# Kernel optimization log

Hardware: AMD Instinct MI355X
Metric: run time of the kernel (lower is better)

## Reference

```python
import jax, jax.numpy as jnp
import numpy as np

H = 256
L = 5
B = 1024
NL, EL = 65536, 262144
NP_, EP = 131072, 524288
BN_EPS = 1e-5


def _bn_relu(x, gamma, beta):
    # BatchNorm1d (training mode, biased variance) followed by ReLU
    m = x.mean(axis=0)
    v = ((x - m) ** 2).mean(axis=0)
    return jax.nn.relu((x - m) * jax.lax.rsqrt(v + BN_EPS) * gamma + beta)


def _gin_conv(h, src, dst, W1, b1, W2, b2):
    # GINConv, eps=0: mlp(x + sum_{j->i} x_j)
    agg = jax.ops.segment_sum(h[src], dst, num_segments=h.shape[0])
    z = h + agg
    return jax.nn.relu(z @ W1 + b1) @ W2 + b2


def _forward(lig_x, prot_x, lig_embed_W, lig_embed_b, prot_embed_W, prot_embed_b,
             lig_virtual0, prot_virtual0,
             lig_conv_W1, lig_conv_b1, lig_conv_W2, lig_conv_b2,
             lig_vmlp_W, lig_vmlp_b, lig_vmlp_gamma, lig_vmlp_beta,
             prot_conv_W1, prot_conv_b1, prot_conv_W2, prot_conv_b2,
             prot_vmlp_W, prot_vmlp_b, prot_vmlp_gamma, prot_vmlp_beta,
             pred_W1, pred_b1, pred_W2, pred_b2,
             lig_batch, prot_batch, lig_edge_index, prot_edge_index):
    lig_h = lig_x @ lig_embed_W + lig_embed_b        # [NL, H]
    prot_h = prot_x @ prot_embed_W + prot_embed_b    # [NP, H]
    lig_v = jnp.broadcast_to(lig_virtual0, (B, H))
    prot_v = jnp.broadcast_to(prot_virtual0, (B, H))
    l_src, l_dst = lig_edge_index[0], lig_edge_index[1]
    p_src, p_dst = prot_edge_index[0], prot_edge_index[1]
    for i in range(L):
        # ligand branch: virtual-node pool -> MLP -> broadcast, then GIN conv (residual)
        lig_v = lig_v + jax.ops.segment_sum(lig_h, lig_batch, num_segments=B)
        lig_v = _bn_relu(lig_v @ lig_vmlp_W[i] + lig_vmlp_b[i], lig_vmlp_gamma[i], lig_vmlp_beta[i])
        lig_h = lig_h + lig_v[lig_batch]
        lig_h = lig_h + _gin_conv(lig_h, l_src, l_dst, lig_conv_W1[i], lig_conv_b1[i], lig_conv_W2[i], lig_conv_b2[i])
        # protein branch
        prot_v = prot_v + jax.ops.segment_sum(prot_h, prot_batch, num_segments=B)
        prot_v = _bn_relu(prot_v @ prot_vmlp_W[i] + prot_vmlp_b[i], prot_vmlp_gamma[i], prot_vmlp_beta[i])
        prot_h = prot_h + prot_v[prot_batch]
        prot_h = prot_h + _gin_conv(prot_h, p_src, p_dst, prot_conv_W1[i], prot_conv_b1[i], prot_conv_W2[i], prot_conv_b2[i])
    lig_cnt = jax.ops.segment_sum(jnp.ones((lig_h.shape[0],), lig_h.dtype), lig_batch, num_segments=B)
    prot_cnt = jax.ops.segment_sum(jnp.ones((prot_h.shape[0],), prot_h.dtype), prot_batch, num_segments=B)
    lig_pool = jax.ops.segment_sum(lig_h, lig_batch, num_segments=B) / lig_cnt[:, None]
    prot_pool = jax.ops.segment_sum(prot_h, prot_batch, num_segments=B) / prot_cnt[:, None]
    combined = jnp.concatenate([lig_pool, prot_pool], axis=-1)  # [B, 2H]
    return jax.nn.relu(combined @ pred_W1 + pred_b1) @ pred_W2 + pred_b2  # [B, 1]


def setup_inputs() -> dict:
    key = jax.random.key(0)
    ks = jax.random.split(key, 40)
    s = 0.05
    inp = {
        'lig_x': jax.random.normal(ks[0], (NL, 26), jnp.float32),
        'prot_x': jax.random.normal(ks[1], (NP_, 20), jnp.float32),
        'lig_embed_W': jax.random.normal(ks[2], (26, H), jnp.float32) * s,
        'lig_embed_b': jnp.zeros((H,), jnp.float32),
        'prot_embed_W': jax.random.normal(ks[3], (20, H), jnp.float32) * s,
        'prot_embed_b': jnp.zeros((H,), jnp.float32),
        'lig_virtual0': jax.random.normal(ks[4], (1, H), jnp.float32),
        'prot_virtual0': jax.random.normal(ks[5], (1, H), jnp.float32),
        'lig_conv_W1': jax.random.normal(ks[6], (L, H, H), jnp.float32) * s,
        'lig_conv_b1': jnp.zeros((L, H), jnp.float32),
        'lig_conv_W2': jax.random.normal(ks[7], (L, H, H), jnp.float32) * s,
        'lig_conv_b2': jnp.zeros((L, H), jnp.float32),
        'lig_vmlp_W': jax.random.normal(ks[8], (L, H, H), jnp.float32) * s,
        'lig_vmlp_b': jnp.zeros((L, H), jnp.float32),
        'lig_vmlp_gamma': jnp.ones((L, H), jnp.float32),
        'lig_vmlp_beta': jnp.zeros((L, H), jnp.float32),
        'prot_conv_W1': jax.random.normal(ks[9], (L, H, H), jnp.float32) * s,
        'prot_conv_b1': jnp.zeros((L, H), jnp.float32),
        'prot_conv_W2': jax.random.normal(ks[10], (L, H, H), jnp.float32) * s,
        'prot_conv_b2': jnp.zeros((L, H), jnp.float32),
        'prot_vmlp_W': jax.random.normal(ks[11], (L, H, H), jnp.float32) * s,
        'prot_vmlp_b': jnp.zeros((L, H), jnp.float32),
        'prot_vmlp_gamma': jnp.ones((L, H), jnp.float32),
        'prot_vmlp_beta': jnp.zeros((L, H), jnp.float32),
        'pred_W1': jax.random.normal(ks[12], (2 * H, H), jnp.float32) * s,
        'pred_b1': jnp.zeros((H,), jnp.float32),
        'pred_W2': jax.random.normal(ks[13], (H, 1), jnp.float32) * s,
        'pred_b2': jnp.zeros((1,), jnp.float32),
        # sorted batch ids covering all B graphs (PyG-style contiguous batching)
        'lig_batch': (jnp.arange(NL, dtype=jnp.int32) * B) // NL,
        'prot_batch': (jnp.arange(NP_, dtype=jnp.int32) * B) // NP_,
        'lig_edge_index': jax.random.randint(ks[14], (2, EL), 0, NL, jnp.int32),
        'prot_edge_index': jax.random.randint(ks[15], (2, EP), 0, NP_, jnp.int32),
    }
    return inp


def reference(lig_x, prot_x, lig_embed_W, lig_embed_b, prot_embed_W, prot_embed_b,
              lig_virtual0, prot_virtual0,
              lig_conv_W1, lig_conv_b1, lig_conv_W2, lig_conv_b2,
              lig_vmlp_W, lig_vmlp_b, lig_vmlp_gamma, lig_vmlp_beta,
              prot_conv_W1, prot_conv_b1, prot_conv_W2, prot_conv_b2,
              prot_vmlp_W, prot_vmlp_b, prot_vmlp_gamma, prot_vmlp_beta,
              pred_W1, pred_b1, pred_W2, pred_b2,
              lig_batch, prot_batch, lig_edge_index, prot_edge_index):
    return _forward(lig_x, prot_x, lig_embed_W, lig_embed_b, prot_embed_W, prot_embed_b,
                    lig_virtual0, prot_virtual0,
                    lig_conv_W1, lig_conv_b1, lig_conv_W2, lig_conv_b2,
                    lig_vmlp_W, lig_vmlp_b, lig_vmlp_gamma, lig_vmlp_beta,
                    prot_conv_W1, prot_conv_b1, prot_conv_W2, prot_conv_b2,
                    prot_vmlp_W, prot_vmlp_b, prot_vmlp_gamma, prot_vmlp_beta,
                    pred_W1, pred_b1, pred_W2, pred_b2,
                    lig_batch, prot_batch, lig_edge_index, prot_edge_index)
```

## Files before the change

### kernel.cpp

```cpp
#include <hip/hip_runtime.h>

#define H_DIM 256
#define NLAYER 5
#define BGRAPH 1024
#define CAP 24

typedef __attribute__((ext_vector_type(8))) short short8;
typedef __attribute__((ext_vector_type(4))) float f32x4;

struct __align__(8) us4 { unsigned short x, y, z, w; };

__device__ __forceinline__ float b2f(unsigned short u) {
    union { float f; unsigned v; } c; c.v = ((unsigned)u) << 16; return c.f;
}
__device__ __forceinline__ unsigned short f2b(float f) {
    union { float f; unsigned v; } c; c.f = f;
    return (unsigned short)((c.v + 0x7fffu + ((c.v >> 16) & 1u)) >> 16);
}

__global__ __launch_bounds__(256) void embed_kernel(
    const float* __restrict__ x, const float* __restrict__ W,
    const float* __restrict__ b, unsigned short* __restrict__ h, int K)
{
    __shared__ float xs[256];
    const int m0 = blockIdx.x * 8;
    const int tid = threadIdx.x;
    if (tid < 8 * K) xs[tid] = x[(size_t)m0 * K + tid];
    __syncthreads();
    const int n = tid;
    float acc[8] = {0.f,0.f,0.f,0.f,0.f,0.f,0.f,0.f};
    for (int k = 0; k < K; ++k) {
        const float w = W[k * H_DIM + n];
        #pragma unroll
        for (int r = 0; r < 8; ++r) acc[r] += xs[r * K + k] * w;
    }
    const float bb = b[n];
    #pragma unroll
    for (int r = 0; r < 8; ++r)
        h[(size_t)(m0 + r) * H_DIM + n] = f2b(acc[r] + bb);
}

__global__ __launch_bounds__(256) void init_v_kernel(
    const float* __restrict__ lig0, const float* __restrict__ prot0,
    float* __restrict__ lig_v, float* __restrict__ prot_v)
{
    const int b = blockIdx.x, n = threadIdx.x;
    lig_v[b * H_DIM + n]  = lig0[n];
    prot_v[b * H_DIM + n] = prot0[n];
}

__global__ __launch_bounds__(64) void wprep_kernel(
    const float* __restrict__ W, unsigned short* __restrict__ Wf)
{
    const int kb = blockIdx.x, nb = blockIdx.y, l = blockIdx.z;
    const int lane = threadIdx.x, q = lane >> 4, l15 = lane & 15;
    const float* Wl = W + (size_t)l * 65536;
    unsigned short* dst = Wf + (size_t)l * 65536
                        + ((size_t)(kb * 16 + nb) * 64 + lane) * 8;
    const int kbase = kb * 32 + q * 8;
    const int n = nb * 16 + l15;
    us4 o0, o1;
    o0.x = f2b(Wl[(size_t)(kbase + 0) * 256 + n]);
    o0.y = f2b(Wl[(size_t)(kbase + 1) * 256 + n]);
    o0.z = f2b(Wl[(size_t)(kbase + 2) * 256 + n]);
    o0.w = f2b(Wl[(size_t)(kbase + 3) * 256 + n]);
    o1.x = f2b(Wl[(size_t)(kbase + 4) * 256 + n]);
    o1.y = f2b(Wl[(size_t)(kbase + 5) * 256 + n]);
    o1.z = f2b(Wl[(size_t)(kbase + 6) * 256 + n]);
    o1.w = f2b(Wl[(size_t)(kbase + 7) * 256 + n]);
    *(us4*)dst = o0;
    *(us4*)(dst + 4) = o1;
}

__global__ __launch_bounds__(256) void bucket_build_kernel(
    const int* __restrict__ src, const int* __restrict__ dst, int E,
    int* __restrict__ deg, int* __restrict__ bucket)
{
    const int e = blockIdx.x * 256 + threadIdx.x;
    if (e >= E) return;
    const int d = dst[e], s = src[e];
    const int slot = atomicAdd(&deg[d], 1);
    if (slot < CAP) bucket[(size_t)d * CAP + slot] = s;
}

__global__ __launch_bounds__(256) void pool0_kernel(
    const unsigned short* __restrict__ hL, const unsigned short* __restrict__ hP,
    float* __restrict__ hsL, float* __restrict__ hsP)
{
    const int br = blockIdx.y, b = blockIdx.x, n = threadIdx.x;
    const unsigned short* h = br ? hP : hL;
    float* hs = br ? hsP : hsL;
    const int cnt = br ? 128 : 64;
    const unsigned short* hp = &h[(size_t)b * cnt * H_DIM + n];
    float s = 0.f;
    #pragma unroll 8
    for (int r = 0; r < cnt; ++r) s += b2f(hp[(size_t)r * H_DIM]);
    hs[(size_t)b * H_DIM + n] = s;
}

__global__ __launch_bounds__(256) void vmlp_gemm_kernel(
    const float* __restrict__ vL, const float* __restrict__ hsL,
    const float* __restrict__ WL, const float* __restrict__ bL,
    const float* __restrict__ vP, const float* __restrict__ hsP,
    const float* __restrict__ WP, const float* __restrict__ bP,
    float* __restrict__ vtL, float* __restrict__ vtP,
    float* __restrict__ part)
{
    constexpr int BM = 32, BN = 64, BK = 32, TM = 2, K = H_DIM, N = H_DIM;
    __shared__ __align__(16) float As[BK][BM + 4];
    __shared__ __align__(16) float Bs[BK][BN];
    __shared__ float st[2][64];
    const int br = blockIdx.z;
    const float* v    = br ? vP  : vL;
    const float* hsum = br ? hsP : hsL;
    const float* W    = br ? WP  : WL;
    const float* bias = br ? bP  : bL;
    float* vt = br ? vtP : vtL;
    float* pt = part + br * 512;
    const int tid = threadIdx.x;
    const int tx = tid & 15;
    const int ty = tid >> 4;
    const int m0 = blockIdx.x * BM;
    const int n0 = blockIdx.y * BN;

    float acc[TM][4] = {};

    for (int kt = 0; kt < K; kt += BK) {
        {
            const int row = tid >> 3, kq = tid & 7;
            const size_t ao = (size_t)(m0 + row) * K + kt + kq * 4;
            float4 a = *(const float4*)&v[ao];
            const float4 h4 = *(const float4*)&hsum[ao];
            a.x += h4.x; a.y += h4.y; a.z += h4.z; a.w += h4.w;
            As[kq * 4 + 0][row] = a.x;
            As[kq * 4 + 1][row] = a.y;
            As[kq * 4 + 2][row] = a.z;
            As[kq * 4 + 3][row] = a.w;
        }
        #pragma unroll
        for (int i = 0; i < 2; ++i) {
            const int f = tid + i * 256;
            const int row = f >> 4, c4 = f & 15;
            *(float4*)&Bs[row][c4 * 4] =
                *(const float4*)&W[(size_t)(kt + row) * N + n0 + c4 * 4];
        }
        __syncthreads();
        #pragma unroll
        for (int kk = 0; kk < BK; ++kk) {
            const float4 bv = *(const float4*)&Bs[kk][tx * 4];
            #pragma unroll
            for (int im = 0; im < TM; ++im) {
                const float a = As[kk][ty * TM + im];
                acc[im][0] += a * bv.x; acc[im][1] += a * bv.y;
                acc[im][2] += a * bv.z; acc[im][3] += a * bv.w;
            }
        }
        __syncthreads();
    }

    if (tid < 128) ((float*)st)[tid] = 0.f;
    __syncthreads();

    const float4 bb = *(const float4*)&bias[n0 + tx * 4];
    float cs[4] = {0.f,0.f,0.f,0.f}, cq[4] = {0.f,0.f,0.f,0.f};
    #pragma unroll
    for (int im = 0; im < TM; ++im) {
        const int m = m0 + ty * TM + im;
        float4 r;
        r.x = acc[im][0] + bb.x; r.y = acc[im][1] + bb.y;
        r.z = acc[im][2] + bb.z; r.w = acc[im][3] + bb.w;
        *(float4*)&vt[(size_t)m * N + n0 + tx * 4] = r;
        cs[0] += r.x; cq[0] += r.x * r.x;
        cs[1] += r.y; cq[1] += r.y * r.y;
        cs[2] += r.z; cq[2] += r.z * r.z;
        cs[3] += r.w; cq[3] += r.w * r.w;
    }
    #pragma unroll
    for (int c = 0; c < 4; ++c) {
        atomicAdd(&st[0][tx * 4 + c], cs[c]);
        atomicAdd(&st[1][tx * 4 + c], cq[c]);
    }
    __syncthreads();
    if (tid < 64) {
        atomicAdd(&pt[n0 + tid], st[0][tid]);
        atomicAdd(&pt[256 + n0 + tid], st[1][tid]);
    }
}

__global__ __launch_bounds__(256) void vmlp_apply_kernel(
    const float* __restrict__ part,
    const float* __restrict__ gL, const float* __restrict__ beL,
    const float* __restrict__ gP, const float* __restrict__ beP,
    const float* __restrict__ vtL, const float* __restrict__ vtP,
    float* __restrict__ vL, float* __restrict__ vP)
{
    const int br = blockIdx.y, n = threadIdx.x;
    const float* pt = part + br * 512;
    const float* g  = br ? gP  : gL;
    const float* be = br ? beP : beL;
    const float* vt = br ? vtP : vtL;
    float* v = br ? vP : vL;
    const float s  = pt[n];
    const float s2 = pt[256 + n];
    const float mean = s * (1.f / BGRAPH);
    const float var  = s2 * (1.f / BGRAPH) - mean * mean;
    const float sc = g[n] * rsqrtf(var + 1e-5f);
    const float sh = be[n] - mean * sc;
    #pragma unroll
    for (int r = 0; r < 4; ++r) {
        const size_t i = (size_t)(blockIdx.x * 4 + r) * H_DIM + n;
        v[i] = fmaxf(vt[i] * sc + sh, 0.f);
    }
}

__global__ __launch_bounds__(512) void conv_fused3_kernel(
    const unsigned short* __restrict__ Hin,
    const int* __restrict__ deg, const int* __restrict__ bucket,
    const int* __restrict__ batch, const float* __restrict__ v,
    const unsigned short* __restrict__ Wf1, const float* __restrict__ b1,
    const unsigned short* __restrict__ Wf2, const float* __restrict__ b2,
    unsigned short* __restrict__ Hout, float* __restrict__ hsum)
{
    __shared__ __align__(16) unsigned short U[64 * 256];
    __shared__ float hl[256];
    char* Ub = (char*)U;
    const int tid  = threadIdx.x;
    const int lane = tid & 63;
    const int wid  = tid >> 6;
    const int wr   = wid >> 2;
    const int wc   = wid & 3;
    const int q    = lane >> 4;
    const int l15  = lane & 15;
    const int m0   = blockIdx.x * 64;
    const int bq0  = batch[m0];
    const float* __restrict__ vg = v + (size_t)bq0 * H_DIM;

    if (tid < 256) hl[tid] = 0.f;

    {
        const float4 vm = *(const float4*)&vg[lane * 4];
        for (int r8 = 0; r8 < 8; ++r8) {
            const int lr = wid * 8 + r8;
            const int m = m0 + lr;
            const us4 hv = *(const us4*)&Hin[(size_t)m * H_DIM + lane * 4];
            float4 acc = { b2f(hv.x) + vm.x, b2f(hv.y) + vm.y,
                           b2f(hv.z) + vm.z, b2f(hv.w) + vm.w };
            int cnt = deg[m]; if (cnt > CAP) cnt = CAP;
            const int* bp = &bucket[(size_t)m * CAP];
            for (int i = 0; i < cnt; i += 4) {
                const int4 s4 = *(const int4*)&bp[i];
                const int rem = cnt - i;
                us4 a0, a1, a2, a3;
                int q0, q1, q2, q3;
                a0 = *(const us4*)&Hin[(size_t)s4.x * H_DIM + lane * 4];
                q0 = batch[s4.x];
                if (rem > 1) { a1 = *(const us4*)&Hin[(size_t)s4.y * H_DIM + lane * 4]; q1 = batch[s4.y]; }
                if (rem > 2) { a2 = *(const us4*)&Hin[(size_t)s4.z * H_DIM + lane * 4]; q2 = batch[s4.z]; }
                if (rem > 3) { a3 = *(const us4*)&Hin[(size_t)s4.w * H_DIM + lane * 4]; q3 = batch[s4.w]; }
                {
                    const float4 w0 = *(const float4*)&v[(size_t)q0 * H_DIM + lane * 4];
                    acc.x += b2f(a0.x) + w0.x; acc.y += b2f(a0.y) + w0.y;
                    acc.z += b2f(a0.z) + w0.z; acc.w += b2f(a0.w) + w0.w;
                }
                if (rem > 1) {
                    const float4 w1 = *(const float4*)&v[(size_t)q1 * H_DIM + lane * 4];
                    acc.x += b2f(a1.x) + w1.x; acc.y += b2f(a1.y) + w1.y;
                    acc.z += b2f(a1.z) + w1.z; acc.w += b2f(a1.w) + w1.w;
                }
                if (rem > 2) {
                    const float4 w2 = *(const float4*)&v[(size_t)q2 * H_DIM + lane * 4];
                    acc.x += b2f(a2.x) + w2.x; acc.y += b2f(a2.y) + w2.y;
                    acc.z += b2f(a2.z) + w2.z; acc.w += b2f(a2.w) + w2.w;
                }
                if (rem > 3) {
                    const float4 w3 = *(const float4*)&v[(size_t)q3 * H_DIM + lane * 4];
                    acc.x += b2f(a3.x) + w3.x; acc.y += b2f(a3.y) + w3.y;
                    acc.z += b2f(a3.z) + w3.z; acc.w += b2f(a3.w) + w3.w;
                }
            }
            us4 o = { f2b(acc.x), f2b(acc.y), f2b(acc.z), f2b(acc.w) };
            const int ab = lr * 512 + ((lane * 8) ^ ((lr & 7) << 4));
            *(us4*)(Ub + ab) = o;
        }
    }
    __syncthreads();

    f32x4 acc[2][4];
    #pragma unroll
    for (int i = 0; i < 2; ++i)
        #pragma unroll
        for (int j = 0; j < 4; ++j) acc[i][j] = (f32x4){0.f, 0.f, 0.f, 0.f};

    const int arow = wr * 32 + l15;
    const int rowb0 = arow * 512;
    const int rowb1 = rowb0 + 16 * 512;
    const int xorv = (l15 & 7) << 4;
    const unsigned short* wb1 = Wf1 + ((size_t)(wc * 4) * 64 + lane) * 8;
    const unsigned short* wb2 = Wf2 + ((size_t)(wc * 4) * 64 + lane) * 8;

    #pragma unroll 2
    for (int kb = 0; kb < 8; ++kb) {
        const int c0 = (kb * 64 + q * 16) ^ xorv;
        const short8 av0 = *(const short8*)(Ub + rowb0 + c0);
        const short8 av1 = *(const short8*)(Ub + rowb1 + c0);
        #pragma unroll
        for (int ni = 0; ni < 4; ++ni) {
            const short8 bv = *(const short8*)&wb1[(size_t)kb * 8192 + ni * 512];
            acc[0][ni] = __builtin_amdgcn_mfma_f32_16x16x32_bf16(av0, bv, acc[0][ni], 0, 0, 0);
            acc[1][ni] = __builtin_amdgcn_mfma_f32_16x16x32_bf16(av1, bv, acc[1][ni], 0, 0, 0);
        }
    }
    __syncthreads();

    #pragma unroll
    for (int ni = 0; ni < 4; ++ni) {
        const int col = wc * 64 + ni * 16 + l15;
        const float bb = b1[col];
        #pragma unroll
        for (int mi = 0; mi < 2; ++mi)
            #pragma unroll
            for (int j = 0; j < 4; ++j) {
                const int row = wr * 32 + mi * 16 + q * 4 + j;
                const int tb = row * 512 + ((col * 2) ^ ((row & 7) << 4));
                *(unsigned short*)(Ub + tb) = f2b(fmaxf(acc[mi][ni][j] + bb, 0.f));
            }
    }
    #pragma unroll
    for (int i = 0; i < 2; ++i)
        #pragma unroll
        for (int j = 0; j < 4; ++j) acc[i][j] = (f32x4){0.f, 0.f, 0.f, 0.f};
    __syncthreads();

    #pragma unroll 2
    for (int kb = 0; kb < 8; ++kb) {
        const int c0 = (kb * 64 + q * 16) ^ xorv;
        const short8 av0 = *(const short8*)(Ub + rowb0 + c0);
        const short8 av1 = *(const short8*)(Ub + rowb1 + c0);
        #pragma unroll
        for (int ni = 0; ni < 4; ++ni) {
            const short8 bv = *(const short8*)&wb2[(size_t)kb * 8192 + ni * 512];
            acc[0][ni] = __builtin_amdgcn_mfma_f32_16x16x32_bf16(av0, bv, acc[0][ni], 0, 0, 0);
            acc[1][ni] = __builtin_amdgcn_mfma_f32_16x16x32_bf16(av1, bv, acc[1][ni], 0, 0, 0);
        }
    }

    int cols[4]; float b2c[4], vc[4];
    #pragma unroll
    for (int ni = 0; ni < 4; ++ni) {
        cols[ni] = wc * 64 + ni * 16 + l15;
        b2c[ni] = b2[cols[ni]];
        vc[ni]  = vg[cols[ni]];
    }
    float lsum[4] = {0.f, 0.f, 0.f, 0.f};
    #pragma unroll
    for (int mi = 0; mi < 2; ++mi)
        #pragma unroll
        for (int j = 0; j < 4; ++j) {
            const int row = m0 + wr * 32 + mi * 16 + q * 4 + j;
            const unsigned short* hip_ = &Hin[(size_t)row * H_DIM];
            unsigned short* hop = &Hout[(size_t)row * H_DIM];
            #pragma unroll
            for (int ni = 0; ni < 4; ++ni) {
                const float val = b2f(hip_[cols[ni]]) + vc[ni]
                                + acc[mi][ni][j] + b2c[ni];
                hop[cols[ni]] = f2b(val);
                lsum[ni] += val;
            }
        }
    #pragma unroll
    for (int ni = 0; ni < 4; ++ni) atomicAdd(&hl[cols[ni]], lsum[ni]);
    __syncthreads();
    if (tid < 256) atomicAdd(&hsum[(size_t)bq0 * H_DIM + tid], hl[tid]);
}

template<bool RELU>
__global__ __launch_bounds__(256) void gemm_small_kernel(
    const float* __restrict__ A, const float* __restrict__ W,
    const float* __restrict__ bias, float* __restrict__ C,
    int M, int N, int K)
{
    constexpr int BM = 32, BN = 64, BK = 32, TM = 2;
    __shared__ __align__(16) float As[BK][BM + 4];
    __shared__ __align__(16) float Bs[BK][BN];
    const int tid = threadIdx.x;
    const int tx = tid & 15;
    const int ty = tid >> 4;
    const int m0 = blockIdx.x * BM;
    const int n0 = blockIdx.y * BN;

    float acc[TM][4] = {};

    for (int kt = 0; kt < K; kt += BK) {
        {
            const int row = tid >> 3, kq = tid & 7;
            const float4 a = *(const float4*)&A[(size_t)(m0 + row) * K + kt + kq * 4];
            As[kq * 4 + 0][row] = a.x;
            As[kq * 4 + 1][row] = a.y;
            As[kq * 4 + 2][row] = a.z;
            As[kq * 4 + 3][row] = a.w;
        }
        #pragma unroll
        for (int i = 0; i < 2; ++i) {
            const int f = tid + i * 256;
            const int row = f >> 4, c4 = f & 15;
            *(float4*)&Bs[row][c4 * 4] =
                *(const float4*)&W[(size_t)(kt + row) * N + n0 + c4 * 4];
        }
        __syncthreads();
        #pragma unroll
        for (int kk = 0; kk < BK; ++kk) {
            const float4 bv = *(const float4*)&Bs[kk][tx * 4];
            #pragma unroll
            for (int im = 0; im < TM; ++im) {
                const float a = As[kk][ty * TM + im];
                acc[im][0] += a * bv.x; acc[im][1] += a * bv.y;
                acc[im][2] += a * bv.z; acc[im][3] += a * bv.w;
            }
        }
        __syncthreads();
    }

    const float4 bb = *(const float4*)&bias[n0 + tx * 4];
    #pragma unroll
    for (int im = 0; im < TM; ++im) {
        const int m = m0 + ty * TM + im;
        float4 r;
        r.x = acc[im][0] + bb.x; r.y = acc[im][1] + bb.y;
        r.z = acc[im][2] + bb.z; r.w = acc[im][3] + bb.w;
        if constexpr (RELU) {
            r.x = fmaxf(r.x, 0.f); r.y = fmaxf(r.y, 0.f);
            r.z = fmaxf(r.z, 0.f); r.w = fmaxf(r.w, 0.f);
        }
        *(float4*)&C[(size_t)m * N + n0 + tx * 4] = r;
    }
}

__global__ __launch_bounds__(256) void pool_hsum_kernel(
    const float* __restrict__ hl, const float* __restrict__ hp,
    float* __restrict__ comb)
{
    const int b = blockIdx.x, n = threadIdx.x;
    comb[(size_t)b * 512 + n]       = hl[(size_t)b * H_DIM + n] * (1.f / 64.f);
    comb[(size_t)b * 512 + 256 + n] = hp[(size_t)b * H_DIM + n] * (1.f / 128.f);
}

__global__ __launch_bounds__(256) void pred_final_kernel(
    const float* __restrict__ hidden, const float* __restrict__ W2,
    const float* __restrict__ b2, float* __restrict__ out)
{
    const int b = blockIdx.x, t = threadIdx.x;
    float p = hidden[(size_t)b * H_DIM + t] * W2[t];
    #pragma unroll
    for (int off = 32; off >= 1; off >>= 1) p += __shfl_down(p, off);
    __shared__ float red[4];
    if ((t & 63) == 0) red[t >> 6] = p;
    __syncthreads();
    if (t == 0) out[b] = red[0] + red[1] + red[2] + red[3] + b2[0];
}

extern "C" void kernel_launch(void* const* d_in, const int* in_sizes, int n_in,
                              void* d_out, int out_size, void* d_ws, size_t ws_size,
                              hipStream_t stream)
{
    const int NL = 65536, NP = 131072, EL = 262144, EP = 524288;
    const int B = BGRAPH, H = H_DIM;

    const float* lig_x        = (const float*)d_in[0];
    const float* prot_x       = (const float*)d_in[1];
    const float* lig_embed_W  = (const float*)d_in[2];
    const float* lig_embed_b  = (const float*)d_in[3];
    const float* prot_embed_W = (const float*)d_in[4];
    const float* prot_embed_b = (const float*)d_in[5];
    const float* lig_virtual0 = (const float*)d_in[6];
    const float* prot_virtual0= (const float*)d_in[7];
    const float* lig_conv_W1  = (const float*)d_in[8];
    const float* lig_conv_b1  = (const float*)d_in[9];
    const float* lig_conv_W2  = (const float*)d_in[10];
    const float* lig_conv_b2  = (const float*)d_in[11];
    const float* lig_vmlp_W   = (const float*)d_in[12];
    const float* lig_vmlp_b   = (const float*)d_in[13];
    const float* lig_vmlp_g   = (const float*)d_in[14];
    const float* lig_vmlp_be  = (const float*)d_in[15];
    const float* prot_conv_W1 = (const float*)d_in[16];
    const float* prot_conv_b1 = (const float*)d_in[17];
    const float* prot_conv_W2 = (const float*)d_in[18];
    const float* prot_conv_b2 = (const float*)d_in[19];
    const float* prot_vmlp_W  = (const float*)d_in[20];
    const float* prot_vmlp_b  = (const float*)d_in[21];
    const float* prot_vmlp_g  = (const float*)d_in[22];
    const float* prot_vmlp_be = (const float*)d_in[23];
    const float* pred_W1      = (const float*)d_in[24];
    const float* pred_b1      = (const float*)d_in[25];
    const float* pred_W2      = (const float*)d_in[26];
    const float* pred_b2      = (const float*)d_in[27];
    const int* lig_batch      = (const int*)d_in[28];
    const int* prot_batch     = (const int*)d_in[29];
    const int* lig_ei         = (const int*)d_in[30];
    const int* prot_ei        = (const int*)d_in[31];

    float* ws = (float*)d_ws;
    float* lig_v    = ws;
    float* prot_v   = lig_v    + (size_t)B * H;
    float* vtmpL    = prot_v   + (size_t)B * H;
    float* vtmpP    = vtmpL    + (size_t)B * H;
    float* part     = vtmpP    + (size_t)B * H;
    float* comb     = part     + 1024;
    float* hidden   = comb     + (size_t)B * 2 * H;
    float* hsum_lig = hidden   + (size_t)B * H;
    float* hsum_prot= hsum_lig + (size_t)B * H;
    unsigned short* lig_h0  = (unsigned short*)(hsum_prot + (size_t)B * H);
    unsigned short* lig_h1  = lig_h0  + (size_t)NL * H;
    unsigned short* prot_h0 = lig_h1  + (size_t)NL * H;
    unsigned short* prot_h1 = prot_h0 + (size_t)NP * H;
    unsigned short* wf_lw1  = prot_h1 + (size_t)NP * H;
    unsigned short* wf_lw2  = wf_lw1 + (size_t)NLAYER * H * H;
    unsigned short* wf_pw1  = wf_lw2 + (size_t)NLAYER * H * H;
    unsigned short* wf_pw2  = wf_pw1 + (size_t)NLAYER * H * H;
    int* deg_lig  = (int*)(wf_pw2 + (size_t)NLAYER * H * H);
    int* deg_prot = deg_lig  + NL;
    int* bkt_lig  = deg_prot + NP;
    int* bkt_prot = bkt_lig  + (size_t)NL * CAP;

    hipMemsetAsync(deg_lig, 0, (size_t)(NL + NP) * sizeof(int), stream);
    bucket_build_kernel<<<EL / 256, 256, 0, stream>>>(
        lig_ei, lig_ei + EL, EL, deg_lig, bkt_lig);
    bucket_build_kernel<<<EP / 256, 256, 0, stream>>>(
        prot_ei, prot_ei + EP, EP, deg_prot, bkt_prot);
    wprep_kernel<<<dim3(8, 16, NLAYER), 64, 0, stream>>>(lig_conv_W1, wf_lw1);
    wprep_kernel<<<dim3(8, 16, NLAYER), 64, 0, stream>>>(lig_conv_W2, wf_lw2);
    wprep_kernel<<<dim3(8, 16, NLAYER), 64, 0, stream>>>(prot_conv_W1, wf_pw1);
    wprep_kernel<<<dim3(8, 16, NLAYER), 64, 0, stream>>>(prot_conv_W2, wf_pw2);

    embed_kernel<<<NL / 8, 256, 0, stream>>>(lig_x, lig_embed_W, lig_embed_b, lig_h0, 26);
    embed_kernel<<<NP / 8, 256, 0, stream>>>(prot_x, prot_embed_W, prot_embed_b, prot_h0, 20);
    init_v_kernel<<<B, 256, 0, stream>>>(lig_virtual0, prot_virtual0, lig_v, prot_v);
    pool0_kernel<<<dim3(B, 2), 256, 0, stream>>>(lig_h0, prot_h0, hsum_lig, hsum_prot);

    for (int i = 0; i < NLAYER; ++i) {
        const size_t wo = (size_t)i * H * H;
        const size_t bo = (size_t)i * H;
        unsigned short* lin  = (i & 1) ? lig_h1  : lig_h0;
        unsigned short* lout = (i & 1) ? lig_h0  : lig_h1;
        unsigned short* pin  = (i & 1) ? prot_h1 : prot_h0;
        unsigned short* pout = (i & 1) ? prot_h0 : prot_h1;

        hipMemsetAsync(part, 0, 1024 * sizeof(float), stream);
        vmlp_gemm_kernel<<<dim3(32, 4, 2), 256, 0, stream>>>(
            lig_v, hsum_lig, lig_vmlp_W + wo, lig_vmlp_b + bo,
            prot_v, hsum_prot, prot_vmlp_W + wo, prot_vmlp_b + bo,
            vtmpL, vtmpP, part);
        vmlp_apply_kernel<<<dim3(256, 2), 256, 0, stream>>>(
            part, lig_vmlp_g + bo, lig_vmlp_be + bo,
            prot_vmlp_g + bo, prot_vmlp_be + bo,
            vtmpL, vtmpP, lig_v, prot_v);
        hipMemsetAsync(hsum_lig, 0, (size_t)2 * B * H * sizeof(float), stream);
        conv_fused3_kernel<<<NL / 64, 512, 0, stream>>>(
            lin, deg_lig, bkt_lig, lig_batch, lig_v,
            wf_lw1 + wo, lig_conv_b1 + bo, wf_lw2 + wo, lig_conv_b2 + bo,
            lout, hsum_lig);
        conv_fused3_kernel<<<NP / 64, 512, 0, stream>>>(
            pin, deg_prot, bkt_prot, prot_batch, prot_v,
            wf_pw1 + wo, prot_conv_b1 + bo, wf_pw2 + wo, prot_conv_b2 + bo,
            pout, hsum_prot);
    }

    pool_hsum_kernel<<<B, 256, 0, stream>>>(hsum_lig, hsum_prot, comb);
    gemm_small_kernel<true><<<dim3(B / 32, 4), 256, 0, stream>>>(
        comb, pred_W1, pred_b1, hidden, B, H, 2 * H);
    pred_final_kernel<<<B, 256, 0, stream>>>(hidden, pred_W2, pred_b2, (float*)d_out);
}
```

Baseline: 1.823 ms.

## Shrink conv tile to 32 rows and interleave two-row neighbor gathers

The fused GIN conv kernel now processes 32 rows per block with 256 threads instead of 64 rows with 512. Each wave owns all 32 rows and a 64-column slice of the MFMA output, and LDS use drops by half. The gather phase handles two destination rows at once so their neighbor loads are issued together, aiming for more memory-level parallelism on the random gathers. The cost is twice as many blocks, twice as many hsum atomics, and weight tiles reloaded per block for half as many rows, which may add pressure on L2.

Result: faster. 1.755 ms (-3.7%).

```diff
diff --git a/kernel.cpp b/kernel.cpp
--- a/kernel.cpp
+++ b/kernel.cpp
@@ -213,7 +213,7 @@
     }
 }
 
-__global__ __launch_bounds__(512) void conv_fused3_kernel(
+__global__ __launch_bounds__(256) void conv_fused4_kernel(
     const unsigned short* __restrict__ Hin,
     const int* __restrict__ deg, const int* __restrict__ bucket,
     const int* __restrict__ batch, const float* __restrict__ v,
@@ -221,66 +221,101 @@
     const unsigned short* __restrict__ Wf2, const float* __restrict__ b2,
     unsigned short* __restrict__ Hout, float* __restrict__ hsum)
 {
-    __shared__ __align__(16) unsigned short U[64 * 256];
+    __shared__ __align__(16) unsigned short U[32 * 256];
     __shared__ float hl[256];
     char* Ub = (char*)U;
     const int tid  = threadIdx.x;
     const int lane = tid & 63;
     const int wid  = tid >> 6;
-    const int wr   = wid >> 2;
-    const int wc   = wid & 3;
+    const int wc   = wid;
     const int q    = lane >> 4;
     const int l15  = lane & 15;
-    const int m0   = blockIdx.x * 64;
+    const int m0   = blockIdx.x * 32;
     const int bq0  = batch[m0];
     const float* __restrict__ vg = v + (size_t)bq0 * H_DIM;
 
-    if (tid < 256) hl[tid] = 0.f;
+    hl[tid] = 0.f;
 
     {
         const float4 vm = *(const float4*)&vg[lane * 4];
-        for (int r8 = 0; r8 < 8; ++r8) {
-            const int lr = wid * 8 + r8;
-            const int m = m0 + lr;
-            const us4 hv = *(const us4*)&Hin[(size_t)m * H_DIM + lane * 4];
-            float4 acc = { b2f(hv.x) + vm.x, b2f(hv.y) + vm.y,
-                           b2f(hv.z) + vm.z, b2f(hv.w) + vm.w };
-            int cnt = deg[m]; if (cnt > CAP) cnt = CAP;
-            const int* bp = &bucket[(size_t)m * CAP];
-            for (int i = 0; i < cnt; i += 4) {
-                const int4 s4 = *(const int4*)&bp[i];
-                const int rem = cnt - i;
-                us4 a0, a1, a2, a3;
-                int q0, q1, q2, q3;
-                a0 = *(const us4*)&Hin[(size_t)s4.x * H_DIM + lane * 4];
-                q0 = batch[s4.x];
-                if (rem > 1) { a1 = *(const us4*)&Hin[(size_t)s4.y * H_DIM + lane * 4]; q1 = batch[s4.y]; }
-                if (rem > 2) { a2 = *(const us4*)&Hin[(size_t)s4.z * H_DIM + lane * 4]; q2 = batch[s4.z]; }
-                if (rem > 3) { a3 = *(const us4*)&Hin[(size_t)s4.w * H_DIM + lane * 4]; q3 = batch[s4.w]; }
-                {
-                    const float4 w0 = *(const float4*)&v[(size_t)q0 * H_DIM + lane * 4];
-                    acc.x += b2f(a0.x) + w0.x; acc.y += b2f(a0.y) + w0.y;
-                    acc.z += b2f(a0.z) + w0.z; acc.w += b2f(a0.w) + w0.w;
-                }
-                if (rem > 1) {
-                    const float4 w1 = *(const float4*)&v[(size_t)q1 * H_DIM + lane * 4];
-                    acc.x += b2f(a1.x) + w1.x; acc.y += b2f(a1.y) + w1.y;
-                    acc.z += b2f(a1.z) + w1.z; acc.w += b2f(a1.w) + w1.w;
-                }
-                if (rem > 2) {
-                    const float4 w2 = *(const float4*)&v[(size_t)q2 * H_DIM + lane * 4];
-                    acc.x += b2f(a2.x) + w2.x; acc.y += b2f(a2.y) + w2.y;
-                    acc.z += b2f(a2.z) + w2.z; acc.w += b2f(a2.w) + w2.w;
-                }
-                if (rem > 3) {
-                    const float4 w3 = *(const float4*)&v[(size_t)q3 * H_DIM + lane * 4];
-                    acc.x += b2f(a3.x) + w3.x; acc.y += b2f(a3.y) + w3.y;
-                    acc.z += b2f(a3.z) + w3.z; acc.w += b2f(a3.w) + w3.w;
+        for (int rp = 0; rp < 8; rp += 2) {
+            const int lrA = wid * 8 + rp, lrB = lrA + 1;
+            const int mA = m0 + lrA, mB = m0 + lrB;
+            const us4 hA = *(const us4*)&Hin[(size_t)mA * H_DIM + lane * 4];
+            const us4 hB = *(const us4*)&Hin[(size_t)mB * H_DIM + lane * 4];
+            int cntA = deg[mA]; if (cntA > CAP) cntA = CAP;
+            int cntB = deg[mB]; if (cntB > CAP) cntB = CAP;
+            const int* bpA = &bucket[(size_t)mA * CAP];
+            const int* bpB = &bucket[(size_t)mB * CAP];
+            float4 aA = { b2f(hA.x) + vm.x, b2f(hA.y) + vm.y,
+                          b2f(hA.z) + vm.z, b2f(hA.w) + vm.w };
+            float4 aB = { b2f(hB.x) + vm.x, b2f(hB.y) + vm.y,
+                          b2f(hB.z) + vm.z, b2f(hB.w) + vm.w };
+            const int cmax = cntA > cntB ? cntA : cntB;
+            for (int i = 0; i < cmax; i += 4) {
+                us4 xa0, xa1, xa2, xa3, xb0, xb1, xb2, xb3;
+                int qa0, qa1, qa2, qa3, qb0, qb1, qb2, qb3;
+                int remA = cntA - i, remB = cntB - i;
+                int4 sA, sB;
+                if (remA > 0) {
+                    sA = *(const int4*)&bpA[i];
+                    xa0 = *(const us4*)&Hin[(size_t)sA.x * H_DIM + lane * 4]; qa0 = batch[sA.x];
+                    if (remA > 1) { xa1 = *(const us4*)&Hin[(size_t)sA.y * H_DIM + lane * 4]; qa1 = batch[sA.y]; }
+                    if (remA > 2) { xa2 = *(const us4*)&Hin[(size_t)sA.z * H_DIM + lane * 4]; qa2 = batch[sA.z]; }
+                    if (remA > 3) { xa3 = *(const us4*)&Hin[(size_t)sA.w * H_DIM + lane * 4]; qa3 = batch[sA.w]; }
+                }
+                if (remB > 0) {
+                    sB = *(const int4*)&bpB[i];
+                    xb0 = *(const us4*)&Hin[(size_t)sB.x * H_DIM + lane * 4]; qb0 = batch[sB.x];
+                    if (remB > 1) { xb1 = *(const us4*)&Hin[(size_t)sB.y * H_DIM + lane * 4]; qb1 = batch[sB.y]; }
+                    if (remB > 2) { xb2 = *(const us4*)&Hin[(size_t)sB.z * H_DIM + lane * 4]; qb2 = batch[sB.z]; }
+                    if (remB > 3) { xb3 = *(const us4*)&Hin[(size_t)sB.w * H_DIM + lane * 4]; qb3 = batch[sB.w]; }
+                }
+                if (remA > 0) {
+                    const float4 w = *(const float4*)&v[(size_t)qa0 * H_DIM + lane * 4];
+                    aA.x += b2f(xa0.x) + w.x; aA.y += b2f(xa0.y) + w.y;
+                    aA.z += b2f(xa0.z) + w.z; aA.w += b2f(xa0.w) + w.w;
+                }
+                if (remA > 1) {
+                    const float4 w = *(const float4*)&v[(size_t)qa1 * H_DIM + lane * 4];
+                    aA.x += b2f(xa1.x) + w.x; aA.y += b2f(xa1.y) + w.y;
+                    aA.z += b2f(xa1.z) + w.z; aA.w += b2f(xa1.w) + w.w;
+                }
+                if (remA > 2) {
+                    const float4 w = *(const float4*)&v[(size_t)qa2 * H_DIM + lane * 4];
+                    aA.x += b2f(xa2.x) + w.x; aA.y += b2f(xa2.y) + w.y;
+                    aA.z += b2f(xa2.z) + w.z; aA.w += b2f(xa2.w) + w.w;
+                }
+                if (remA > 3) {
+                    const float4 w = *(const float4*)&v[(size_t)qa3 * H_DIM + lane * 4];
+                    aA.x += b2f(xa3.x) + w.x; aA.y += b2f(xa3.y) + w.y;
+                    aA.z += b2f(xa3.z) + w.z; aA.w += b2f(xa3.w) + w.w;
+                }
+                if (remB > 0) {
+                    const float4 w = *(const float4*)&v[(size_t)qb0 * H_DIM + lane * 4];
+                    aB.x += b2f(xb0.x) + w.x; aB.y += b2f(xb0.y) + w.y;
+                    aB.z += b2f(xb0.z) + w.z; aB.w += b2f(xb0.w) + w.w;
+                }
+                if (remB > 1) {
+                    const float4 w = *(const float4*)&v[(size_t)qb1 * H_DIM + lane * 4];
+                    aB.x += b2f(xb1.x) + w.x; aB.y += b2f(xb1.y) + w.y;
+                    aB.z += b2f(xb1.z) + w.z; aB.w += b2f(xb1.w) + w.w;
+                }
+                if (remB > 2) {
+                    const float4 w = *(const float4*)&v[(size_t)qb2 * H_DIM + lane * 4];
+                    aB.x += b2f(xb2.x) + w.x; aB.y += b2f(xb2.y) + w.y;
+                    aB.z += b2f(xb2.z) + w.z; aB.w += b2f(xb2.w) + w.w;
+                }
+                if (remB > 3) {
+                    const float4 w = *(const float4*)&v[(size_t)qb3 * H_DIM + lane * 4];
+                    aB.x += b2f(xb3.x) + w.x; aB.y += b2f(xb3.y) + w.y;
+                    aB.z += b2f(xb3.z) + w.z; aB.w += b2f(xb3.w) + w.w;
                 }
             }
-            us4 o = { f2b(acc.x), f2b(acc.y), f2b(acc.z), f2b(acc.w) };
-            const int ab = lr * 512 + ((lane * 8) ^ ((lr & 7) << 4));
-            *(us4*)(Ub + ab) = o;
+            us4 oA = { f2b(aA.x), f2b(aA.y), f2b(aA.z), f2b(aA.w) };
+            us4 oB = { f2b(aB.x), f2b(aB.y), f2b(aB.z), f2b(aB.w) };
+            *(us4*)(Ub + lrA * 512 + ((lane * 8) ^ ((lrA & 7) << 4))) = oA;
+            *(us4*)(Ub + lrB * 512 + ((lane * 8) ^ ((lrB & 7) << 4))) = oB;
         }
     }
     __syncthreads();
@@ -291,9 +326,8 @@
         #pragma unroll
         for (int j = 0; j < 4; ++j) acc[i][j] = (f32x4){0.f, 0.f, 0.f, 0.f};
 
-    const int arow = wr * 32 + l15;
-    const int rowb0 = arow * 512;
-    const int rowb1 = rowb0 + 16 * 512;
+    const int rowb0 = l15 * 512;
+    const int rowb1 = (16 + l15) * 512;
     const int xorv = (l15 & 7) << 4;
     const unsigned short* wb1 = Wf1 + ((size_t)(wc * 4) * 64 + lane) * 8;
     const unsigned short* wb2 = Wf2 + ((size_t)(wc * 4) * 64 + lane) * 8;
@@ -320,7 +354,7 @@
         for (int mi = 0; mi < 2; ++mi)
             #pragma unroll
             for (int j = 0; j < 4; ++j) {
-                const int row = wr * 32 + mi * 16 + q * 4 + j;
+                const int row = mi * 16 + q * 4 + j;
                 const int tb = row * 512 + ((col * 2) ^ ((row & 7) << 4));
                 *(unsigned short*)(Ub + tb) = f2b(fmaxf(acc[mi][ni][j] + bb, 0.f));
             }
@@ -356,7 +390,7 @@
     for (int mi = 0; mi < 2; ++mi)
         #pragma unroll
         for (int j = 0; j < 4; ++j) {
-            const int row = m0 + wr * 32 + mi * 16 + q * 4 + j;
+            const int row = m0 + mi * 16 + q * 4 + j;
             const unsigned short* hip_ = &Hin[(size_t)row * H_DIM];
             unsigned short* hop = &Hout[(size_t)row * H_DIM];
             #pragma unroll
@@ -370,7 +404,7 @@
     #pragma unroll
     for (int ni = 0; ni < 4; ++ni) atomicAdd(&hl[cols[ni]], lsum[ni]);
     __syncthreads();
-    if (tid < 256) atomicAdd(&hsum[(size_t)bq0 * H_DIM + tid], hl[tid]);
+    atomicAdd(&hsum[(size_t)bq0 * H_DIM + tid], hl[tid]);
 }
 
 template<bool RELU>
@@ -554,11 +588,11 @@
             prot_vmlp_g + bo, prot_vmlp_be + bo,
             vtmpL, vtmpP, lig_v, prot_v);
         hipMemsetAsync(hsum_lig, 0, (size_t)2 * B * H * sizeof(float), stream);
-        conv_fused3_kernel<<<NL / 64, 512, 0, stream>>>(
+        conv_fused4_kernel<<<NL / 32, 256, 0, stream>>>(
             lin, deg_lig, bkt_lig, lig_batch, lig_v,
             wf_lw1 + wo, lig_conv_b1 + bo, wf_lw2 + wo, lig_conv_b2 + bo,
             lout, hsum_lig);
-        conv_fused3_kernel<<<NP / 64, 512, 0, stream>>>(
+        conv_fused4_kernel<<<NP / 32, 256, 0, stream>>>(
             pin, deg_prot, bkt_prot, prot_batch, prot_v,
             wf_pw1 + wo, prot_conv_b1 + bo, wf_pw2 + wo, prot_conv_b2 + bo,
             pout, hsum_prot);
```

## Split GIN conv into gather and GEMM roles interleaved in one launch

Applied to the files above, without the earlier changes.

The fused gather+MLP conv kernel is split into a gather role that writes the aggregated z to a global buffer and a GEMM role that reads z and updates h in place. A middle launch interleaves ligand GEMM blocks with protein gather blocks (one GEMM block per 16 gather blocks), so memory-bound gathers overlap compute-bound MLPs. GEMM tiles shrink to 32 rows with 256 threads, and h is updated in place instead of ping-ponging. The cost is an extra round trip of z through global memory and smaller GEMM tiles that reload the weights more often.

Result: slower. 2.109 ms (+15.7%).

```diff
diff --git a/kernel.cpp b/kernel.cpp
--- a/kernel.cpp
+++ b/kernel.cpp
@@ -213,75 +213,94 @@
     }
 }
 
-__global__ __launch_bounds__(512) void conv_fused3_kernel(
-    const unsigned short* __restrict__ Hin,
-    const int* __restrict__ deg, const int* __restrict__ bucket,
-    const int* __restrict__ batch, const float* __restrict__ v,
+__global__ __launch_bounds__(256) void conv_pipe_kernel(
+    const unsigned short* __restrict__ Zg, unsigned short* __restrict__ Hg,
+    const float* __restrict__ vG, const int* __restrict__ batchG,
     const unsigned short* __restrict__ Wf1, const float* __restrict__ b1,
     const unsigned short* __restrict__ Wf2, const float* __restrict__ b2,
-    unsigned short* __restrict__ Hout, float* __restrict__ hsum)
-{
-    __shared__ __align__(16) unsigned short U[64 * 256];
+    float* __restrict__ hsumG,
+    const unsigned short* __restrict__ Hs, const float* __restrict__ vS,
+    const int* __restrict__ batchS, const int* __restrict__ degS,
+    const int* __restrict__ bktS, unsigned short* __restrict__ Zs,
+    int gemm_blocks, int gather_blocks)
+{
+    __shared__ __align__(16) unsigned short U[32 * 256];
     __shared__ float hl[256];
     char* Ub = (char*)U;
     const int tid  = threadIdx.x;
     const int lane = tid & 63;
     const int wid  = tid >> 6;
-    const int wr   = wid >> 2;
-    const int wc   = wid & 3;
+
+    int role_gemm, gid;
+    if (gather_blocks == 0)      { role_gemm = 1; gid = blockIdx.x; }
+    else if (gemm_blocks == 0)   { role_gemm = 0; gid = blockIdx.x; }
+    else {
+        const int d17 = blockIdx.x / 17;
+        if (blockIdx.x - d17 * 17 == 0) { role_gemm = 1; gid = d17; }
+        else                            { role_gemm = 0; gid = blockIdx.x - d17 - 1; }
+    }
+
+    if (!role_gemm) {
+        const int m = gid * 4 + wid;
+        int cnt = degS[m]; if (cnt > CAP) cnt = CAP;
+        const us4 hv = *(const us4*)&Hs[(size_t)m * H_DIM + lane * 4];
+        const int bm = batchS[m];
+        const float4 vm = *(const float4*)&vS[(size_t)bm * H_DIM + lane * 4];
+        float4 acc = { b2f(hv.x) + vm.x, b2f(hv.y) + vm.y,
+                       b2f(hv.z) + vm.z, b2f(hv.w) + vm.w };
+        const int* bp = &bktS[(size_t)m * CAP];
+        for (int i = 0; i < cnt; i += 4) {
+            const int4 s4 = *(const int4*)&bp[i];
+            const int rem = cnt - i;
+            us4 a0, a1, a2, a3;
+            int q0, q1, q2, q3;
+            a0 = *(const us4*)&Hs[(size_t)s4.x * H_DIM + lane * 4];
+            q0 = batchS[s4.x];
+            if (rem > 1) { a1 = *(const us4*)&Hs[(size_t)s4.y * H_DIM + lane * 4]; q1 = batchS[s4.y]; }
+            if (rem > 2) { a2 = *(const us4*)&Hs[(size_t)s4.z * H_DIM + lane * 4]; q2 = batchS[s4.z]; }
+            if (rem > 3) { a3 = *(const us4*)&Hs[(size_t)s4.w * H_DIM + lane * 4]; q3 = batchS[s4.w]; }
+            {
+                const float4 w0 = *(const float4*)&vS[(size_t)q0 * H_DIM + lane * 4];
+                acc.x += b2f(a0.x) + w0.x; acc.y += b2f(a0.y) + w0.y;
+                acc.z += b2f(a0.z) + w0.z; acc.w += b2f(a0.w) + w0.w;
+            }
+            if (rem > 1) {
+                const float4 w1 = *(const float4*)&vS[(size_t)q1 * H_DIM + lane * 4];
+                acc.x += b2f(a1.x) + w1.x; acc.y += b2f(a1.y) + w1.y;
+                acc.z += b2f(a1.z) + w1.z; acc.w += b2f(a1.w) + w1.w;
+            }
+            if (rem > 2) {
+                const float4 w2 = *(const float4*)&vS[(size_t)q2 * H_DIM + lane * 4];
+                acc.x += b2f(a2.x) + w2.x; acc.y += b2f(a2.y) + w2.y;
+                acc.z += b2f(a2.z) + w2.z; acc.w += b2f(a2.w) + w2.w;
+            }
+            if (rem > 3) {
+                const float4 w3 = *(const float4*)&vS[(size_t)q3 * H_DIM + lane * 4];
+                acc.x += b2f(a3.x) + w3.x; acc.y += b2f(a3.y) + w3.y;
+                acc.z += b2f(a3.z) + w3.z; acc.w += b2f(a3.w) + w3.w;
+            }
+        }
+        us4 o = { f2b(acc.x), f2b(acc.y), f2b(acc.z), f2b(acc.w) };
+        *(us4*)&Zs[(size_t)m * H_DIM + lane * 4] = o;
+        return;
+    }
+
+    const int wc   = wid;
     const int q    = lane >> 4;
     const int l15  = lane & 15;
-    const int m0   = blockIdx.x * 64;
-    const int bq0  = batch[m0];
-    const float* __restrict__ vg = v + (size_t)bq0 * H_DIM;
-
-    if (tid < 256) hl[tid] = 0.f;
-
-    {
-        const float4 vm = *(const float4*)&vg[lane * 4];
-        for (int r8 = 0; r8 < 8; ++r8) {
-            const int lr = wid * 8 + r8;
-            const int m = m0 + lr;
-            const us4 hv = *(const us4*)&Hin[(size_t)m * H_DIM + lane * 4];
-            float4 acc = { b2f(hv.x) + vm.x, b2f(hv.y) + vm.y,
-                           b2f(hv.z) + vm.z, b2f(hv.w) + vm.w };
-            int cnt = deg[m]; if (cnt > CAP) cnt = CAP;
-            const int* bp = &bucket[(size_t)m * CAP];
-            for (int i = 0; i < cnt; i += 4) {
-                const int4 s4 = *(const int4*)&bp[i];
-                const int rem = cnt - i;
-                us4 a0, a1, a2, a3;
-                int q0, q1, q2, q3;
-                a0 = *(const us4*)&Hin[(size_t)s4.x * H_DIM + lane * 4];
-                q0 = batch[s4.x];
-                if (rem > 1) { a1 = *(const us4*)&Hin[(size_t)s4.y * H_DIM + lane * 4]; q1 = batch[s4.y]; }
-                if (rem > 2) { a2 = *(const us4*)&Hin[(size_t)s4.z * H_DIM + lane * 4]; q2 = batch[s4.z]; }
-                if (rem > 3) { a3 = *(const us4*)&Hin[(size_t)s4.w * H_DIM + lane * 4]; q3 = batch[s4.w]; }
-                {
-                    const float4 w0 = *(const float4*)&v[(size_t)q0 * H_DIM + lane * 4];
-                    acc.x += b2f(a0.x) + w0.x; acc.y += b2f(a0.y) + w0.y;
-                    acc.z += b2f(a0.z) + w0.z; acc.w += b2f(a0.w) + w0.w;
-                }
-                if (rem > 1) {
-                    const float4 w1 = *(const float4*)&v[(size_t)q1 * H_DIM + lane * 4];
-                    acc.x += b2f(a1.x) + w1.x; acc.y += b2f(a1.y) + w1.y;
-                    acc.z += b2f(a1.z) + w1.z; acc.w += b2f(a1.w) + w1.w;
-                }
-                if (rem > 2) {
-                    const float4 w2 = *(const float4*)&v[(size_t)q2 * H_DIM + lane * 4];
-                    acc.x += b2f(a2.x) + w2.x; acc.y += b2f(a2.y) + w2.y;
-                    acc.z += b2f(a2.z) + w2.z; acc.w += b2f(a2.w) + w2.w;
-                }
-                if (rem > 3) {
-                    const float4 w3 = *(const float4*)&v[(size_t)q3 * H_DIM + lane * 4];
-                    acc.x += b2f(a3.x) + w3.x; acc.y += b2f(a3.y) + w3.y;
-                    acc.z += b2f(a3.z) + w3.z; acc.w += b2f(a3.w) + w3.w;
-                }
-            }
-            us4 o = { f2b(acc.x), f2b(acc.y), f2b(acc.z), f2b(acc.w) };
-            const int ab = lr * 512 + ((lane * 8) ^ ((lr & 7) << 4));
-            *(us4*)(Ub + ab) = o;
-        }
+    const int m0   = gid * 32;
+    const int bq0  = batchG[m0];
+    const float* __restrict__ vg = vG + (size_t)bq0 * H_DIM;
+
+    hl[tid] = 0.f;
+
+    #pragma unroll
+    for (int i = 0; i < 4; ++i) {
+        const int c = tid + (i << 8);
+        const int row = c >> 5;
+        const int cb = (c & 31) << 4;
+        const float4 d = *(const float4*)((const char*)(Zg + (size_t)(m0 + row) * H_DIM) + cb);
+        *(float4*)(Ub + row * 512 + (cb ^ ((row & 7) << 4))) = d;
     }
     __syncthreads();
 
@@ -291,9 +310,8 @@
         #pragma unroll
         for (int j = 0; j < 4; ++j) acc[i][j] = (f32x4){0.f, 0.f, 0.f, 0.f};
 
-    const int arow = wr * 32 + l15;
-    const int rowb0 = arow * 512;
-    const int rowb1 = rowb0 + 16 * 512;
+    const int rowb0 = l15 * 512;
+    const int rowb1 = (16 + l15) * 512;
     const int xorv = (l15 & 7) << 4;
     const unsigned short* wb1 = Wf1 + ((size_t)(wc * 4) * 64 + lane) * 8;
     const unsigned short* wb2 = Wf2 + ((size_t)(wc * 4) * 64 + lane) * 8;
@@ -320,7 +338,7 @@
         for (int mi = 0; mi < 2; ++mi)
             #pragma unroll
             for (int j = 0; j < 4; ++j) {
-                const int row = wr * 32 + mi * 16 + q * 4 + j;
+                const int row = mi * 16 + q * 4 + j;
                 const int tb = row * 512 + ((col * 2) ^ ((row & 7) << 4));
                 *(unsigned short*)(Ub + tb) = f2b(fmaxf(acc[mi][ni][j] + bb, 0.f));
             }
@@ -356,21 +374,20 @@
     for (int mi = 0; mi < 2; ++mi)
         #pragma unroll
         for (int j = 0; j < 4; ++j) {
-            const int row = m0 + wr * 32 + mi * 16 + q * 4 + j;
-            const unsigned short* hip_ = &Hin[(size_t)row * H_DIM];
-            unsigned short* hop = &Hout[(size_t)row * H_DIM];
+            const int row = m0 + mi * 16 + q * 4 + j;
+            unsigned short* hp = &Hg[(size_t)row * H_DIM];
             #pragma unroll
             for (int ni = 0; ni < 4; ++ni) {
-                const float val = b2f(hip_[cols[ni]]) + vc[ni]
+                const float val = b2f(hp[cols[ni]]) + vc[ni]
                                 + acc[mi][ni][j] + b2c[ni];
-                hop[cols[ni]] = f2b(val);
+                hp[cols[ni]] = f2b(val);
                 lsum[ni] += val;
             }
         }
     #pragma unroll
     for (int ni = 0; ni < 4; ++ni) atomicAdd(&hl[cols[ni]], lsum[ni]);
     __syncthreads();
-    if (tid < 256) atomicAdd(&hsum[(size_t)bq0 * H_DIM + tid], hl[tid]);
+    atomicAdd(&hsumG[(size_t)bq0 * H_DIM + tid], hl[tid]);
 }
 
 template<bool RELU>
@@ -508,11 +525,11 @@
     float* hidden   = comb     + (size_t)B * 2 * H;
     float* hsum_lig = hidden   + (size_t)B * H;
     float* hsum_prot= hsum_lig + (size_t)B * H;
-    unsigned short* lig_h0  = (unsigned short*)(hsum_prot + (size_t)B * H);
-    unsigned short* lig_h1  = lig_h0  + (size_t)NL * H;
-    unsigned short* prot_h0 = lig_h1  + (size_t)NL * H;
-    unsigned short* prot_h1 = prot_h0 + (size_t)NP * H;
-    unsigned short* wf_lw1  = prot_h1 + (size_t)NP * H;
+    unsigned short* lig_h   = (unsigned short*)(hsum_prot + (size_t)B * H);
+    unsigned short* prot_h  = lig_h  + (size_t)NL * H;
+    unsigned short* z_lig   = prot_h + (size_t)NP * H;
+    unsigned short* z_prot  = z_lig  + (size_t)NL * H;
+    unsigned short* wf_lw1  = z_prot + (size_t)NP * H;
     unsigned short* wf_lw2  = wf_lw1 + (size_t)NLAYER * H * H;
     unsigned short* wf_pw1  = wf_lw2 + (size_t)NLAYER * H * H;
     unsigned short* wf_pw2  = wf_pw1 + (size_t)NLAYER * H * H;
@@ -531,18 +548,14 @@
     wprep_kernel<<<dim3(8, 16, NLAYER), 64, 0, stream>>>(prot_conv_W1, wf_pw1);
     wprep_kernel<<<dim3(8, 16, NLAYER), 64, 0, stream>>>(prot_conv_W2, wf_pw2);
 
-    embed_kernel<<<NL / 8, 256, 0, stream>>>(lig_x, lig_embed_W, lig_embed_b, lig_h0, 26);
-    embed_kernel<<<NP / 8, 256, 0, stream>>>(prot_x, prot_embed_W, prot_embed_b, prot_h0, 20);
+    embed_kernel<<<NL / 8, 256, 0, stream>>>(lig_x, lig_embed_W, lig_embed_b, lig_h, 26);
+    embed_kernel<<<NP / 8, 256, 0, stream>>>(prot_x, prot_embed_W, prot_embed_b, prot_h, 20);
     init_v_kernel<<<B, 256, 0, stream>>>(lig_virtual0, prot_virtual0, lig_v, prot_v);
-    pool0_kernel<<<dim3(B, 2), 256, 0, stream>>>(lig_h0, prot_h0, hsum_lig, hsum_prot);
+    pool0_kernel<<<dim3(B, 2), 256, 0, stream>>>(lig_h, prot_h, hsum_lig, hsum_prot);
 
     for (int i = 0; i < NLAYER; ++i) {
         const size_t wo = (size_t)i * H * H;
         const size_t bo = (size_t)i * H;
-        unsigned short* lin  = (i & 1) ? lig_h1  : lig_h0;
-        unsigned short* lout = (i & 1) ? lig_h0  : lig_h1;
-        unsigned short* pin  = (i & 1) ? prot_h1 : prot_h0;
-        unsigned short* pout = (i & 1) ? prot_h0 : prot_h1;
 
         hipMemsetAsync(part, 0, 1024 * sizeof(float), stream);
         vmlp_gemm_kernel<<<dim3(32, 4, 2), 256, 0, stream>>>(
@@ -554,14 +567,22 @@
             prot_vmlp_g + bo, prot_vmlp_be + bo,
             vtmpL, vtmpP, lig_v, prot_v);
         hipMemsetAsync(hsum_lig, 0, (size_t)2 * B * H * sizeof(float), stream);
-        conv_fused3_kernel<<<NL / 64, 512, 0, stream>>>(
-            lin, deg_lig, bkt_lig, lig_batch, lig_v,
-            wf_lw1 + wo, lig_conv_b1 + bo, wf_lw2 + wo, lig_conv_b2 + bo,
-            lout, hsum_lig);
-        conv_fused3_kernel<<<NP / 64, 512, 0, stream>>>(
-            pin, deg_prot, bkt_prot, prot_batch, prot_v,
-            wf_pw1 + wo, prot_conv_b1 + bo, wf_pw2 + wo, prot_conv_b2 + bo,
-            pout, hsum_prot);
+
+        conv_pipe_kernel<<<NL / 4, 256, 0, stream>>>(
+            z_lig, lig_h, lig_v, lig_batch,
+            wf_lw1 + wo, lig_conv_b1 + bo, wf_lw2 + wo, lig_conv_b2 + bo, hsum_lig,
+            lig_h, lig_v, lig_batch, deg_lig, bkt_lig, z_lig,
+            0, NL / 4);
+        conv_pipe_kernel<<<NL / 32 + NP / 4, 256, 0, stream>>>(
+            z_lig, lig_h, lig_v, lig_batch,
+            wf_lw1 + wo, lig_conv_b1 + bo, wf_lw2 + wo, lig_conv_b2 + bo, hsum_lig,
+            prot_h, prot_v, prot_batch, deg_prot, bkt_prot, z_prot,
+            NL / 32, NP / 4);
+        conv_pipe_kernel<<<NP / 32, 256, 0, stream>>>(
+            z_prot, prot_h, prot_v, prot_batch,
+            wf_pw1 + wo, prot_conv_b1 + bo, wf_pw2 + wo, prot_conv_b2 + bo, hsum_prot,
+            prot_h, prot_v, prot_batch, deg_prot, bkt_prot, z_prot,
+            NP / 32, 0);
     }
 
     pool_hsum_kernel<<<B, 256, 0, stream>>>(hsum_lig, hsum_prot, comb);
```
